# Kernel tuning notes

Measured on AMD Instinct MI355X. Metric: run time of the kernel, lower is better.

## Reference

```python
import jax, jax.numpy as jnp
import numpy as np

B, C, H, W = 4, 256, 256, 256
P = 256            # num_points
THRESH = 0.8
EPS = 1e-5


def setup_inputs() -> dict:
    key = jax.random.key(0)
    ks = jax.random.split(key, 4)
    x = jax.random.normal(ks[0], (B, C, H, W), dtype=jnp.float32)
    edge = jax.random.uniform(ks[1], (B, 1, H, W), dtype=jnp.float32)
    # GCN params (Conv1d kernel_size=1, no bias) + eval-mode BatchNorm params
    w_adj = jax.random.normal(ks[2], (P, P), dtype=jnp.float32) * (1.0 / np.sqrt(P))
    w_wg = jax.random.normal(ks[3], (C, C), dtype=jnp.float32) * (1.0 / np.sqrt(C))
    return {
        "x": x, "edge": edge,
        "w_adj": w_adj,
        "g_adj": jnp.ones((P,), jnp.float32), "b_adj": jnp.zeros((P,), jnp.float32),
        "m_adj": jnp.zeros((P,), jnp.float32), "v_adj": jnp.ones((P,), jnp.float32),
        "w_wg": w_wg,
        "g_wg": jnp.ones((C,), jnp.float32), "b_wg": jnp.zeros((C,), jnp.float32),
        "m_wg": jnp.zeros((C,), jnp.float32), "v_wg": jnp.ones((C,), jnp.float32),
    }


def _bn(z, mean, var, gamma, beta):
    # eval-mode BatchNorm1d over axis 1 of (B, ch, L)
    inv = gamma / jnp.sqrt(var + EPS)
    return z * inv[None, :, None] + (beta - mean * inv)[None, :, None]


def reference(x, edge, w_adj, g_adj, b_adj, m_adj, v_adj,
              w_wg, g_wg, b_wg, m_wg, v_wg):
    Bx, Cx, Hx, Wx = x.shape
    HW = Hx * Wx
    # threshold boundary map, pick P most-uncertain grid points per image
    e = jnp.where(edge < THRESH, 0.0, edge).reshape(Bx, HW)
    _, idx = jax.lax.top_k(e, P)                      # (B, P) int32 indices into HW
    xf = x.reshape(Bx, Cx, HW)
    idx3 = jnp.broadcast_to(idx[:, None, :], (Bx, Cx, P))
    feat = jnp.take_along_axis(xf, idx3, axis=2)      # gather: (B, C, P)
    feat = feat.transpose(0, 2, 1)                    # (B, P, C) = (b, n, d)
    # GCN stage 1: adjacency mix over nodes + BN + ReLU + residual
    z = jnp.einsum('ij,bjd->bid', w_adj, feat)        # (B, P, C)
    z = jax.nn.relu(_bn(z, m_adj, v_adj, g_adj, b_adj)) + feat
    # GCN stage 2: feature transform + BN + ReLU
    zt = z.transpose(0, 2, 1)                         # (B, C, P)
    z2 = jnp.einsum('cd,bdp->bcp', w_wg, zt)          # (B, C, P)
    z2 = jax.nn.relu(_bn(z2, m_wg, v_wg, g_wg, b_wg))
    # scatter reasoned point features back into the grid (indices are unique per row)
    bi = jnp.arange(Bx)[:, None, None]
    ci = jnp.arange(Cx)[None, :, None]
    out = xf.at[bi, ci, idx3].set(z2)
    return out.reshape(Bx, Cx, Hx, Wx)
```

## Files before the change

### kernel.cpp

```cpp
#include <hip/hip_runtime.h>
#include <stdint.h>

#define HW_   65536
#define B_    4
#define C_    256
#define P_    256
#define TH_   0.8f
#define EPS_  1e-5f

__device__ __forceinline__ uint64_t make_key(const float* __restrict__ edge, int b, int i) {
    float v = edge[b * HW_ + i];
    if (v < TH_) v = 0.0f;
    uint32_t fb = __float_as_uint(v);
    return ((uint64_t)fb << 32) | (uint32_t)(65535 - i);
}

__global__ __launch_bounds__(1024) void topk_kernel(const float* __restrict__ edge,
                                                    int* __restrict__ idx_out) {
    const int b = blockIdx.x;
    const int tid = threadIdx.x;
    __shared__ unsigned int hist[256];
    __shared__ int s_digit;
    __shared__ unsigned int s_above;
    __shared__ unsigned int s_cnt;
    __shared__ uint64_t skeys[256];

    uint64_t prefix = 0, mask = 0;
    int k = P_;
    for (int shift = 56; shift >= 0; shift -= 8) {
        if (tid < 256) hist[tid] = 0;
        __syncthreads();
        for (int s = 0; s < HW_ / 1024; ++s) {
            int i = tid + s * 1024;
            uint64_t key = make_key(edge, b, i);
            if ((key & mask) == prefix)
                atomicAdd(&hist[(unsigned)(key >> shift) & 255u], 1u);
        }
        __syncthreads();
        if (tid == 0) {
            unsigned int c = 0;
            int d = 255;
            for (; d > 0; --d) {
                unsigned int h = hist[d];
                if (c + h >= (unsigned)k) break;
                c += h;
            }
            s_digit = d;
            s_above = c;
        }
        __syncthreads();
        k -= (int)s_above;
        prefix |= ((uint64_t)(unsigned)s_digit) << shift;
        mask   |= (255ull << shift);
        __syncthreads();
    }

    if (tid == 0) s_cnt = 0;
    __syncthreads();
    for (int s = 0; s < HW_ / 1024; ++s) {
        int i = tid + s * 1024;
        uint64_t key = make_key(edge, b, i);
        if (key >= prefix) {
            unsigned int pos = atomicAdd(&s_cnt, 1u);
            if (pos < 256u) skeys[pos] = key;
        }
    }
    __syncthreads();

    for (int kk = 2; kk <= 256; kk <<= 1) {
        for (int j = kk >> 1; j > 0; j >>= 1) {
            if (tid < 256) {
                int ixj = tid ^ j;
                if (ixj > tid) {
                    uint64_t a = skeys[tid], c2 = skeys[ixj];
                    bool desc = ((tid & kk) == 0);
                    if (desc ? (a < c2) : (a > c2)) { skeys[tid] = c2; skeys[ixj] = a; }
                }
            }
            __syncthreads();
        }
    }
    if (tid < 256) idx_out[b * P_ + tid] = 65535 - (int)(skeys[tid] & 0xFFFFFFFFull);
}

__global__ __launch_bounds__(256) void gather_kernel(const float* __restrict__ x,
                                                     const int* __restrict__ idx,
                                                     float* __restrict__ feat) {
    const int bn = blockIdx.x;
    const int d = threadIdx.x;
    const int b = bn >> 8;
    const int hw = idx[bn];
    feat[(size_t)bn * C_ + d] = x[((size_t)(b * C_ + d)) * HW_ + hw];
}

__global__ __launch_bounds__(256) void mm1_kernel(const float* __restrict__ w_adj,
                                                  const float* __restrict__ feat,
                                                  const float* __restrict__ g,
                                                  const float* __restrict__ bb,
                                                  const float* __restrict__ m,
                                                  const float* __restrict__ vv,
                                                  float* __restrict__ z) {
    __shared__ __align__(16) float a_s[64][68];
    __shared__ __align__(16) float b_s[64][68];
    const int b = blockIdx.y;
    const int i0 = (blockIdx.x >> 2) * 64;
    const int d0 = (blockIdx.x & 3) * 64;
    const int tid = threadIdx.x;
    const int tx = tid & 15, ty = tid >> 4;
    const float* fb = feat + (size_t)b * P_ * C_;

    float acc[4][4] = {};
    for (int k0 = 0; k0 < 256; k0 += 64) {
        for (int l = tid; l < 4096; l += 256) {
            int r = l >> 6, c = l & 63;
            a_s[r][c] = w_adj[(i0 + r) * 256 + (k0 + c)];
            b_s[r][c] = fb[(size_t)(k0 + r) * 256 + (d0 + c)];
        }
        __syncthreads();
        #pragma unroll
        for (int kk = 0; kk < 64; kk += 4) {
            float4 a4[4], b4[4];
            #pragma unroll
            for (int r = 0; r < 4; ++r) a4[r] = *(const float4*)&a_s[ty * 4 + r][kk];
            #pragma unroll
            for (int j = 0; j < 4; ++j) b4[j] = *(const float4*)&b_s[kk + j][tx * 4];
            #pragma unroll
            for (int r = 0; r < 4; ++r) {
                const float4 av = a4[r];
                const float aj0 = av.x, aj1 = av.y, aj2 = av.z, aj3 = av.w;
                acc[r][0] = fmaf(aj0, b4[0].x, acc[r][0]);
                acc[r][1] = fmaf(aj0, b4[0].y, acc[r][1]);
                acc[r][2] = fmaf(aj0, b4[0].z, acc[r][2]);
                acc[r][3] = fmaf(aj0, b4[0].w, acc[r][3]);
                acc[r][0] = fmaf(aj1, b4[1].x, acc[r][0]);
                acc[r][1] = fmaf(aj1, b4[1].y, acc[r][1]);
                acc[r][2] = fmaf(aj1, b4[1].z, acc[r][2]);
                acc[r][3] = fmaf(aj1, b4[1].w, acc[r][3]);
                acc[r][0] = fmaf(aj2, b4[2].x, acc[r][0]);
                acc[r][1] = fmaf(aj2, b4[2].y, acc[r][1]);
                acc[r][2] = fmaf(aj2, b4[2].z, acc[r][2]);
                acc[r][3] = fmaf(aj2, b4[2].w, acc[r][3]);
                acc[r][0] = fmaf(aj3, b4[3].x, acc[r][0]);
                acc[r][1] = fmaf(aj3, b4[3].y, acc[r][1]);
                acc[r][2] = fmaf(aj3, b4[3].z, acc[r][2]);
                acc[r][3] = fmaf(aj3, b4[3].w, acc[r][3]);
            }
        }
        __syncthreads();
    }
    #pragma unroll
    for (int r = 0; r < 4; ++r) {
        const int i = i0 + ty * 4 + r;
        const float inv = g[i] / sqrtf(vv[i] + EPS_);
        const float beta = bb[i] - m[i] * inv;
        const int d = d0 + tx * 4;
        float4 res = *(const float4*)&fb[(size_t)i * 256 + d];
        float4 o;
        o.x = fmaxf(acc[r][0] * inv + beta, 0.0f) + res.x;
        o.y = fmaxf(acc[r][1] * inv + beta, 0.0f) + res.y;
        o.z = fmaxf(acc[r][2] * inv + beta, 0.0f) + res.z;
        o.w = fmaxf(acc[r][3] * inv + beta, 0.0f) + res.w;
        *(float4*)&z[((size_t)b * P_ + i) * C_ + d] = o;
    }
}

__global__ __launch_bounds__(256) void mm2_kernel(const float* __restrict__ w_wg,
                                                  const float* __restrict__ z,
                                                  const int* __restrict__ idx,
                                                  const float* __restrict__ g,
                                                  const float* __restrict__ bb,
                                                  const float* __restrict__ m,
                                                  const float* __restrict__ vv,
                                                  float* __restrict__ out) {
    __shared__ __align__(16) float a_s[64][68];
    __shared__ __align__(16) float bt_s[64][68];
    const int b = blockIdx.y;
    const int c0 = (blockIdx.x >> 2) * 64;
    const int p0 = (blockIdx.x & 3) * 64;
    const int tid = threadIdx.x;
    const int tx = tid & 15, ty = tid >> 4;
    const float* zb = z + (size_t)b * P_ * C_;

    float acc[4][4] = {};
    for (int k0 = 0; k0 < 256; k0 += 64) {
        for (int l = tid; l < 4096; l += 256) {
            int r = l >> 6, c = l & 63;
            a_s[r][c] = w_wg[(c0 + r) * 256 + (k0 + c)];
            bt_s[c][r] = zb[(size_t)(p0 + r) * 256 + (k0 + c)];
        }
        __syncthreads();
        #pragma unroll
        for (int kk = 0; kk < 64; kk += 4) {
            float4 a4[4], b4[4];
            #pragma unroll
            for (int r = 0; r < 4; ++r) a4[r] = *(const float4*)&a_s[ty * 4 + r][kk];
            #pragma unroll
            for (int j = 0; j < 4; ++j) b4[j] = *(const float4*)&bt_s[kk + j][tx * 4];
            #pragma unroll
            for (int r = 0; r < 4; ++r) {
                const float4 av = a4[r];
                const float aj0 = av.x, aj1 = av.y, aj2 = av.z, aj3 = av.w;
                acc[r][0] = fmaf(aj0, b4[0].x, acc[r][0]);
                acc[r][1] = fmaf(aj0, b4[0].y, acc[r][1]);
                acc[r][2] = fmaf(aj0, b4[0].z, acc[r][2]);
                acc[r][3] = fmaf(aj0, b4[0].w, acc[r][3]);
                acc[r][0] = fmaf(aj1, b4[1].x, acc[r][0]);
                acc[r][1] = fmaf(aj1, b4[1].y, acc[r][1]);
                acc[r][2] = fmaf(aj1, b4[1].z, acc[r][2]);
                acc[r][3] = fmaf(aj1, b4[1].w, acc[r][3]);
                acc[r][0] = fmaf(aj2, b4[2].x, acc[r][0]);
                acc[r][1] = fmaf(aj2, b4[2].y, acc[r][1]);
                acc[r][2] = fmaf(aj2, b4[2].z, acc[r][2]);
                acc[r][3] = fmaf(aj2, b4[2].w, acc[r][3]);
                acc[r][0] = fmaf(aj3, b4[3].x, acc[r][0]);
                acc[r][1] = fmaf(aj3, b4[3].y, acc[r][1]);
                acc[r][2] = fmaf(aj3, b4[3].z, acc[r][2]);
                acc[r][3] = fmaf(aj3, b4[3].w, acc[r][3]);
            }
        }
        __syncthreads();
    }
    int pidx[4];
    #pragma unroll
    for (int cc = 0; cc < 4; ++cc) pidx[cc] = idx[b * P_ + p0 + tx * 4 + cc];
    #pragma unroll
    for (int r = 0; r < 4; ++r) {
        const int c = c0 + ty * 4 + r;
        const float inv = g[c] / sqrtf(vv[c] + EPS_);
        const float beta = bb[c] - m[c] * inv;
        float* orow = out + ((size_t)(b * C_ + c)) * HW_;
        #pragma unroll
        for (int cc = 0; cc < 4; ++cc) {
            orow[pidx[cc]] = fmaxf(acc[r][cc] * inv + beta, 0.0f);
        }
    }
}

extern "C" void kernel_launch(void* const* d_in, const int* in_sizes, int n_in,
                              void* d_out, int out_size, void* d_ws, size_t ws_size,
                              hipStream_t stream) {
    const float* x     = (const float*)d_in[0];
    const float* edge  = (const float*)d_in[1];
    const float* w_adj = (const float*)d_in[2];
    const float* g_a   = (const float*)d_in[3];
    const float* b_a   = (const float*)d_in[4];
    const float* m_a   = (const float*)d_in[5];
    const float* v_a   = (const float*)d_in[6];
    const float* w_wg  = (const float*)d_in[7];
    const float* g_w   = (const float*)d_in[8];
    const float* b_w   = (const float*)d_in[9];
    const float* m_w   = (const float*)d_in[10];
    const float* v_w   = (const float*)d_in[11];
    float* out = (float*)d_out;

    char* ws = (char*)d_ws;
    int*   idx  = (int*)ws;
    float* feat = (float*)(ws + 4096);
    float* z    = (float*)(ws + 4096 + (size_t)B_ * P_ * C_ * 4);

    hipMemcpyAsync(out, x, (size_t)B_ * C_ * HW_ * sizeof(float),
                   hipMemcpyDeviceToDevice, stream);

    topk_kernel<<<B_, 1024, 0, stream>>>(edge, idx);

    gather_kernel<<<B_ * P_, 256, 0, stream>>>(x, idx, feat);

    mm1_kernel<<<dim3(16, B_), 256, 0, stream>>>(w_adj, feat, g_a, b_a, m_a, v_a, z);

    mm2_kernel<<<dim3(16, B_), 256, 0, stream>>>(w_wg, z, idx, g_w, b_w, m_w, v_w, out);
}
```

Baseline: 711.3 us.

## Replace single-block radix-select top-k with chunked bitonic sort and merge

Replaces the 4-block radix-select top-k, which makes eight full passes over each image's edge map, with a two-stage scheme. The first stage has 16 blocks per image, each bitonic-sorting a 4096-element chunk in shared memory and keeping its top 256 keys. A merge kernel then bitonic-sorts the 4096 candidates per image. The hipMemcpyAsync device-to-device copy of x into out is also replaced by a grid-stride float4 copy kernel. The merge step is still a single block per image and needs 32KB of shared memory. The large copy (about 268MB) likely dominates total time, so the gain depends on how the copy kernel compares with the runtime memcpy.

```diff
diff --git a/kernel.cpp b/kernel.cpp
--- a/kernel.cpp
+++ b/kernel.cpp
@@ -8,79 +8,69 @@
 #define TH_   0.8f
 #define EPS_  1e-5f
 
-__device__ __forceinline__ uint64_t make_key(const float* __restrict__ edge, int b, int i) {
-    float v = edge[b * HW_ + i];
+#define CHUNK_  4096
+#define NCHUNK_ (HW_ / CHUNK_)
+#define NCAND_  (NCHUNK_ * P_)
+
+__device__ __forceinline__ uint64_t make_key(float v, int i) {
     if (v < TH_) v = 0.0f;
-    uint32_t fb = __float_as_uint(v);
-    return ((uint64_t)fb << 32) | (uint32_t)(65535 - i);
-}
-
-__global__ __launch_bounds__(1024) void topk_kernel(const float* __restrict__ edge,
-                                                    int* __restrict__ idx_out) {
+    return ((uint64_t)__float_as_uint(v) << 32) | (uint32_t)(65535 - i);
+}
+
+__global__ __launch_bounds__(512) void topk_local_kernel(const float* __restrict__ edge,
+                                                         uint64_t* __restrict__ cand) {
+    __shared__ uint64_t sk[CHUNK_];
+    const int b = blockIdx.y;
+    const int chunk = blockIdx.x;
+    const int tid = threadIdx.x;
+    const int base = chunk * CHUNK_;
+    for (int t = tid; t < CHUNK_; t += 512) {
+        const int i = base + t;
+        sk[t] = make_key(edge[b * HW_ + i], i);
+    }
+    __syncthreads();
+    for (int k = 2; k <= CHUNK_; k <<= 1) {
+        for (int j = k >> 1; j > 0; j >>= 1) {
+            for (int t = tid; t < CHUNK_ / 2; t += 512) {
+                const int i = 2 * t - (t & (j - 1));
+                const int ixj = i + j;
+                const uint64_t a = sk[i], c = sk[ixj];
+                const bool desc = ((i & k) == 0);
+                if (desc ? (a < c) : (a > c)) { sk[i] = c; sk[ixj] = a; }
+            }
+            __syncthreads();
+        }
+    }
+    if (tid < 256) cand[(b * NCHUNK_ + chunk) * P_ + tid] = sk[tid];
+}
+
+__global__ __launch_bounds__(1024) void topk_merge_kernel(const uint64_t* __restrict__ cand,
+                                                          int* __restrict__ idx_out) {
+    __shared__ uint64_t sk[NCAND_];
     const int b = blockIdx.x;
     const int tid = threadIdx.x;
-    __shared__ unsigned int hist[256];
-    __shared__ int s_digit;
-    __shared__ unsigned int s_above;
-    __shared__ unsigned int s_cnt;
-    __shared__ uint64_t skeys[256];
-
-    uint64_t prefix = 0, mask = 0;
-    int k = P_;
-    for (int shift = 56; shift >= 0; shift -= 8) {
-        if (tid < 256) hist[tid] = 0;
-        __syncthreads();
-        for (int s = 0; s < HW_ / 1024; ++s) {
-            int i = tid + s * 1024;
-            uint64_t key = make_key(edge, b, i);
-            if ((key & mask) == prefix)
-                atomicAdd(&hist[(unsigned)(key >> shift) & 255u], 1u);
-        }
-        __syncthreads();
-        if (tid == 0) {
-            unsigned int c = 0;
-            int d = 255;
-            for (; d > 0; --d) {
-                unsigned int h = hist[d];
-                if (c + h >= (unsigned)k) break;
-                c += h;
-            }
-            s_digit = d;
-            s_above = c;
-        }
-        __syncthreads();
-        k -= (int)s_above;
-        prefix |= ((uint64_t)(unsigned)s_digit) << shift;
-        mask   |= (255ull << shift);
-        __syncthreads();
-    }
-
-    if (tid == 0) s_cnt = 0;
+    for (int t = tid; t < NCAND_; t += 1024) sk[t] = cand[b * NCAND_ + t];
     __syncthreads();
-    for (int s = 0; s < HW_ / 1024; ++s) {
-        int i = tid + s * 1024;
-        uint64_t key = make_key(edge, b, i);
-        if (key >= prefix) {
-            unsigned int pos = atomicAdd(&s_cnt, 1u);
-            if (pos < 256u) skeys[pos] = key;
-        }
-    }
-    __syncthreads();
-
-    for (int kk = 2; kk <= 256; kk <<= 1) {
-        for (int j = kk >> 1; j > 0; j >>= 1) {
-            if (tid < 256) {
-                int ixj = tid ^ j;
-                if (ixj > tid) {
-                    uint64_t a = skeys[tid], c2 = skeys[ixj];
-                    bool desc = ((tid & kk) == 0);
-                    if (desc ? (a < c2) : (a > c2)) { skeys[tid] = c2; skeys[ixj] = a; }
-                }
+    for (int k = 2; k <= NCAND_; k <<= 1) {
+        for (int j = k >> 1; j > 0; j >>= 1) {
+            for (int t = tid; t < NCAND_ / 2; t += 1024) {
+                const int i = 2 * t - (t & (j - 1));
+                const int ixj = i + j;
+                const uint64_t a = sk[i], c = sk[ixj];
+                const bool desc = ((i & k) == 0);
+                if (desc ? (a < c) : (a > c)) { sk[i] = c; sk[ixj] = a; }
             }
             __syncthreads();
         }
     }
-    if (tid < 256) idx_out[b * P_ + tid] = 65535 - (int)(skeys[tid] & 0xFFFFFFFFull);
+    if (tid < 256) idx_out[b * P_ + tid] = 65535 - (int)(sk[tid] & 0xFFFFFFFFull);
+}
+
+__global__ __launch_bounds__(256) void copy_kernel(const float4* __restrict__ src,
+                                                   float4* __restrict__ dst, int n4) {
+    int i = blockIdx.x * 256 + threadIdx.x;
+    const int stride = gridDim.x * 256;
+    for (; i < n4; i += stride) dst[i] = src[i];
 }
 
 __global__ __launch_bounds__(256) void gather_kernel(const float* __restrict__ x,
@@ -254,14 +244,16 @@
     float* out = (float*)d_out;
 
     char* ws = (char*)d_ws;
-    int*   idx  = (int*)ws;
-    float* feat = (float*)(ws + 4096);
-    float* z    = (float*)(ws + 4096 + (size_t)B_ * P_ * C_ * 4);
-
-    hipMemcpyAsync(out, x, (size_t)B_ * C_ * HW_ * sizeof(float),
-                   hipMemcpyDeviceToDevice, stream);
-
-    topk_kernel<<<B_, 1024, 0, stream>>>(edge, idx);
+    int*      idx  = (int*)ws;
+    uint64_t* cand = (uint64_t*)(ws + 4096);
+    float*    feat = (float*)(ws + 4096 + (size_t)B_ * NCAND_ * 8);
+    float*    z    = feat + (size_t)B_ * P_ * C_;
+
+    copy_kernel<<<4096, 256, 0, stream>>>((const float4*)x, (float4*)out,
+                                          (int)((size_t)B_ * C_ * HW_ / 4));
+
+    topk_local_kernel<<<dim3(NCHUNK_, B_), 512, 0, stream>>>(edge, cand);
+    topk_merge_kernel<<<B_, 1024, 0, stream>>>(cand, idx);
 
     gather_kernel<<<B_ * P_, 256, 0, stream>>>(x, idx, feat);
 
```

Measured after the change: 615.8 us. -13.4%, faster.
